# Kernel optimization log

Measured on AMD Instinct MI355X. Metric: run time of the kernel, lower is better.

The kernel has to match this reference:

```python
import jax, jax.numpy as jnp
import numpy as np

N, E, F_IN, HID, L, G = 50000, 400000, 128, 64, 3, 512
HEADS = 4  # per-head dim C = HID = 64 (PyG TransformerConv: out_channels per head)


def setup_inputs() -> dict:
    key = jax.random.key(0)
    ks = jax.random.split(key, 16)
    x = jax.random.normal(ks[0], (N, F_IN), dtype=jnp.float32)
    edge_index = jax.random.randint(ks[1], (2, E), 0, N, dtype=jnp.int64)
    batch = jnp.sort(jax.random.randint(ks[2], (N,), 0, G, dtype=jnp.int64))
    s_in = 1.0 / np.sqrt(F_IN)
    s_h = 1.0 / np.sqrt(HID)
    lin0_w = jax.random.normal(ks[3], (F_IN, HID), dtype=jnp.float32) * s_in
    lin0_b = jnp.zeros((HID,), dtype=jnp.float32)
    # stacked per-layer params [L, ...]
    Wq = jax.random.normal(ks[4], (L, HID, HEADS * HID), dtype=jnp.float32) * s_h
    Wk = jax.random.normal(ks[5], (L, HID, HEADS * HID), dtype=jnp.float32) * s_h
    Wv = jax.random.normal(ks[6], (L, HID, HEADS * HID), dtype=jnp.float32) * s_h
    bq = jnp.zeros((L, HEADS * HID), dtype=jnp.float32)
    bk = jnp.zeros((L, HEADS * HID), dtype=jnp.float32)
    bv = jnp.zeros((L, HEADS * HID), dtype=jnp.float32)
    Ws = jax.random.normal(ks[7], (L, HID, HID), dtype=jnp.float32) * s_h
    bs = jnp.zeros((L, HID), dtype=jnp.float32)
    return {"x": x, "edge_index": edge_index, "batch": batch,
            "lin0_w": lin0_w, "lin0_b": lin0_b,
            "Wq": Wq, "bq": bq, "Wk": Wk, "bk": bk, "Wv": Wv, "bv": bv,
            "Ws": Ws, "bs": bs}


def _transformer_conv(h, src, dst, Wq, bq, Wk, bk, Wv, bv, Ws, bs):
    n = h.shape[0]
    C = Wq.shape[1] // HEADS
    q = (h @ Wq + bq).reshape(n, HEADS, C)
    k = (h @ Wk + bk).reshape(n, HEADS, C)
    v = (h @ Wv + bv).reshape(n, HEADS, C)
    # per-edge attention logits: query at dst, key at src  -> [E, H]
    scale = jnp.asarray(1.0 / np.sqrt(C), h.dtype)
    logits = jnp.einsum('ehc,ehc->eh', q[dst], k[src]) * scale
    # segment softmax over incoming edges of each destination node
    m = jax.ops.segment_max(logits, dst, num_segments=n)
    e = jnp.exp(logits - m[dst])
    denom = jax.ops.segment_sum(e, dst, num_segments=n)
    p = e / denom[dst]  # every edge's dst segment is nonempty
    agg = jax.ops.segment_sum(p[:, :, None] * v[src], dst, num_segments=n)  # [n,H,C]
    return agg.mean(axis=1) + h @ Ws + bs  # concat=False: head mean + root skip


def reference(x, edge_index, batch, lin0_w, lin0_b, Wq, bq, Wk, bk, Wv, bv, Ws, bs):
    src, dst = edge_index[0], edge_index[1]
    h = x @ lin0_w + lin0_b  # [N, HID]; dropout is identity in eval mode
    for l in range(L):
        h = jax.nn.relu(_transformer_conv(h, src, dst, Wq[l], bq[l], Wk[l], bk[l],
                                          Wv[l], bv[l], Ws[l], bs[l]))
    # global add pool over graphs
    return jax.ops.segment_sum(h, batch, num_segments=G)  # [G, HID]
```

## Files before the change

### kernel.cpp

```cpp
#include <hip/hip_runtime.h>
#include <math.h>

#define F_IN 128
#define HID 64
#define NLAYER 3
#define QSW 832
#define QS_ROW 320
#define KV_ROW 512

typedef unsigned short ushort_t;
typedef __bf16 bf16x8 __attribute__((ext_vector_type(8)));
typedef unsigned short u16x8 __attribute__((ext_vector_type(8)));
typedef float f32x4 __attribute__((ext_vector_type(4)));
typedef float f32x2 __attribute__((ext_vector_type(2)));

__device__ __forceinline__ ushort_t f2bf(float f) {
  unsigned u = __float_as_uint(f);
  u += 0x7fffu + ((u >> 16) & 1u);
  return (ushort_t)(u >> 16);
}
__device__ __forceinline__ float bf2f(ushort_t s) {
  return __uint_as_float(((unsigned)s) << 16);
}
__device__ __forceinline__ float blo(unsigned u) { return __uint_as_float(u << 16); }
__device__ __forceinline__ float bhi(unsigned u) { return __uint_as_float(u & 0xffff0000u); }

__device__ __forceinline__ void dec8v(unsigned lo, unsigned hi, f32x2* f) {
  f[0] = __builtin_amdgcn_cvt_pk_f32_fp8((int)lo, false);
  f[1] = __builtin_amdgcn_cvt_pk_f32_fp8((int)lo, true);
  f[2] = __builtin_amdgcn_cvt_pk_f32_fp8((int)hi, false);
  f[3] = __builtin_amdgcn_cvt_pk_f32_fp8((int)hi, true);
}

__global__ __launch_bounds__(256) void aux_k(const int* __restrict__ dst, int* __restrict__ cnt,
                                             int* __restrict__ rank, int e, int nbE,
                                             const float* __restrict__ Wq, const float* __restrict__ Wk,
                                             const float* __restrict__ Wv, const float* __restrict__ Ws,
                                             const float* __restrict__ w0, const float* __restrict__ b0,
                                             const float* __restrict__ bq, const float* __restrict__ bk,
                                             const float* __restrict__ bv, const float* __restrict__ bs,
                                             ushort_t* __restrict__ wp0, ushort_t* __restrict__ wp12,
                                             float* __restrict__ bp,
                                             float* __restrict__ out, int out_size) {
  __shared__ float w0s[128 * 64];
  int blk = blockIdx.x;
  int t = threadIdx.x;
  if (blk < 105) {
    int b = blk * 4 + (t >> 6);
    int lane = t & 63;
    if (blk < 52) {
#pragma unroll
      for (int i = 0; i < 8; i++) {
        int idx = (t + i * 256) * 4;
        *(float4*)&w0s[idx] = *(const float4*)(w0 + idx);
      }
      __syncthreads();
      int ntg = b >> 2, kt = b & 3;
      int col = ntg * 16 + (lane & 15);
      int kb = kt * 32 + (lane >> 4) * 8;
      const float* W; int c, stride;
      if (col < 256)      { W = Wq; c = col;       stride = 256; }
      else if (col < 512) { W = Wk; c = col - 256; stride = 256; }
      else if (col < 768) { W = Wv; c = col - 512; stride = 256; }
      else                { W = Ws; c = col - 768; stride = 64; }
      float vals[8] = {0.f, 0.f, 0.f, 0.f, 0.f, 0.f, 0.f, 0.f};
#pragma unroll 4
      for (int j = 0; j < 64; j++) {
        float wj = W[(long long)j * stride + c];
#pragma unroll
        for (int ee = 0; ee < 8; ee++) vals[ee] = fmaf(w0s[(kb + ee) * 64 + j], wj, vals[ee]);
      }
      ushort_t* p = wp0 + ((long long)b * 64 + lane) * 8;
      ushort4 lo{f2bf(vals[0]), f2bf(vals[1]), f2bf(vals[2]), f2bf(vals[3])};
      ushort4 hi{f2bf(vals[4]), f2bf(vals[5]), f2bf(vals[6]), f2bf(vals[7])};
      *(ushort4*)p = lo;
      *(ushort4*)(p + 4) = hi;
    } else if (b < 416) {
      int idx = b - 208;
      int l = 1 + idx / 104, tt = idx % 104;
      int ntg = tt >> 1, kt = tt & 1;
      int col = ntg * 16 + (lane & 15);
      int kb = kt * 32 + (lane >> 4) * 8;
      const float* W; int c, stride;
      if (col < 256)      { W = Wq + (long long)l * 64 * 256; c = col;       stride = 256; }
      else if (col < 512) { W = Wk + (long long)l * 64 * 256; c = col - 256; stride = 256; }
      else if (col < 768) { W = Wv + (long long)l * 64 * 256; c = col - 512; stride = 256; }
      else                { W = Ws + (long long)l * 64 * 64;  c = col - 768; stride = 64; }
      float vals[8];
#pragma unroll
      for (int ee = 0; ee < 8; ee++) vals[ee] = W[(long long)(kb + ee) * stride + c];
      ushort_t* p = wp12 + (long long)(l - 1) * (104 * 512) + ((long long)tt * 64 + lane) * 8;
      ushort4 lo{f2bf(vals[0]), f2bf(vals[1]), f2bf(vals[2]), f2bf(vals[3])};
      ushort4 hi{f2bf(vals[4]), f2bf(vals[5]), f2bf(vals[6]), f2bf(vals[7])};
      *(ushort4*)p = lo;
      *(ushort4*)(p + 4) = hi;
    } else if (b < 419) {
      int l = b - 416;
      if (l == 0) {
        float b0v = b0[lane];
        for (int c = lane; c < QSW; c += 64) {
          const float* W; const float* borig; int cc, stride;
          if (c < 256)      { W = Wq; borig = bq; cc = c;       stride = 256; }
          else if (c < 512) { W = Wk; borig = bk; cc = c - 256; stride = 256; }
          else if (c < 768) { W = Wv; borig = bv; cc = c - 512; stride = 256; }
          else              { W = Ws; borig = bs; cc = c - 768; stride = 64; }
          float acc = borig[cc];
#pragma unroll 4
          for (int j = 0; j < 64; j++)
            acc = fmaf(__shfl(b0v, j), W[(long long)j * stride + cc], acc);
          bp[c] = acc;
        }
      } else {
        for (int c = lane; c < QSW; c += 64) {
          float v = (c < 256) ? bq[l * 256 + c]
                  : (c < 512) ? bk[l * 256 + c - 256]
                  : (c < 768) ? bv[l * 256 + c - 512]
                  : bs[l * 64 + c - 768];
          bp[l * QSW + c] = v;
        }
      }
    }
    return;
  }
  blk -= 105;
  if (blk < nbE) {
    int i = blk * 256 + t;
    if (i < e) rank[i] = atomicAdd(&cnt[dst[i]], 1);
    return;
  }
  blk -= nbE;
  int zi = blk * 256 + t;
  if (zi * 4 + 3 < out_size) {
    *(float4*)(out + zi * 4) = float4{0.f, 0.f, 0.f, 0.f};
  } else {
    for (int c = zi * 4; c < out_size; c++) out[c] = 0.f;
  }
}

__global__ __launch_bounds__(1024) void scan_block_k(const int* __restrict__ cnt, int* __restrict__ excl,
                                                     int* __restrict__ bsum, int n) {
  __shared__ int wsum[16];
  int t = threadIdx.x;
  int wv = t >> 6, lane = t & 63;
  int i = blockIdx.x * 1024 + t;
  int orig = (i < n) ? cnt[i] : 0;
  int v = orig;
#pragma unroll
  for (int off = 1; off < 64; off <<= 1) {
    int u = __shfl_up(v, off);
    if (lane >= off) v += u;
  }
  if (lane == 63) wsum[wv] = v;
  __syncthreads();
  if (t < 16) {
    int s = wsum[t];
    int s2 = s;
#pragma unroll
    for (int off = 1; off < 16; off <<= 1) {
      int u = __shfl_up(s2, off);
      if (t >= off) s2 += u;
    }
    wsum[t] = s2 - s;
  }
  __syncthreads();
  int base = wsum[wv];
  if (i < n) excl[i] = base + v - orig;
  if (t == 1023) bsum[blockIdx.x] = base + v;
}

__global__ __launch_bounds__(256) void scatter_rowptr_k(const int* __restrict__ src, const int* __restrict__ dst,
                                                        const int* __restrict__ excl, const int* __restrict__ bsum,
                                                        const int* __restrict__ rank, int* __restrict__ rowp,
                                                        int* __restrict__ srt, int n, int e, int nb) {
  __shared__ int sb[64];
  int t = threadIdx.x;
  if (t < 64) {
    int orig = (t < nb) ? bsum[t] : 0;
    int v = orig;
#pragma unroll
    for (int off = 1; off < 64; off <<= 1) {
      int u = __shfl_up(v, off);
      if (t >= off) v += u;
    }
    sb[t] = v - orig;
  }
  __syncthreads();
  int i = blockIdx.x * 256 + t;
  if (i < n) rowp[i] = excl[i] + sb[i >> 10];
  if (i == 0) rowp[n] = e;
  if (i < e) {
    int d = dst[i];
    srt[excl[d] + sb[d >> 10] + rank[i]] = src[i];
  }
}

#define QS_STR 328
#define KV_STR 528
template <int K, int AF32>
__global__ __launch_bounds__(256) void gemm_fused(const void* __restrict__ Av, const ushort_t* __restrict__ Wp,
                                                  const float* __restrict__ bias, ushort_t* __restrict__ Cq,
                                                  unsigned char* __restrict__ Ckv, int n) {
  constexpr int KT = K / 32;
  __shared__ ushort_t qs_lds[32][QS_STR];
  __shared__ unsigned char kv_lds[32][KV_STR];
  int tid = threadIdx.x;
  int lane = tid & 63;
  int wv = __builtin_amdgcn_readfirstlane((int)(tid >> 6));
  int m0 = blockIdx.x * 32;
  int lr = lane & 15, lq = lane >> 4;

  bf16x8 a[2][KT];
#pragma unroll
  for (int mr = 0; mr < 2; mr++) {
    int row = m0 + mr * 16 + lr;
    if (row >= n) row = n - 1;
    if constexpr (AF32) {
      const float* Af = (const float*)Av;
#pragma unroll
      for (int kt = 0; kt < KT; kt++) {
        const float* p = Af + (long long)row * K + kt * 32 + lq * 8;
        float4 f0 = *(const float4*)p;
        float4 f1 = *(const float4*)(p + 4);
        u16x8 u;
        u[0] = f2bf(f0.x); u[1] = f2bf(f0.y); u[2] = f2bf(f0.z); u[3] = f2bf(f0.w);
        u[4] = f2bf(f1.x); u[5] = f2bf(f1.y); u[6] = f2bf(f1.z); u[7] = f2bf(f1.w);
        a[mr][kt] = __builtin_bit_cast(bf16x8, u);
      }
    } else {
      const ushort_t* Ab = (const ushort_t*)Av;
#pragma unroll
      for (int kt = 0; kt < KT; kt++)
        a[mr][kt] = *(const bf16x8*)(Ab + (long long)row * K + kt * 32 + lq * 8);
    }
  }
  int ntg0 = wv * 13;
  bf16x8 bw[KT];
  bf16x8 bwn[KT];
#pragma unroll
  for (int kt = 0; kt < KT; kt++)
    bw[kt] = *(const bf16x8*)(Wp + ((long long)(ntg0 * KT + kt) * 64 + lane) * 8);
  float4 b4 = *(const float4*)(bias + ntg0 * 16 + lq * 4);
#pragma unroll 1
  for (int t = 0; t < 13; t++) {
    int ntg = ntg0 + t;
    float4 b4n;
    if (t < 12) {
#pragma unroll
      for (int kt = 0; kt < KT; kt++)
        bwn[kt] = *(const bf16x8*)(Wp + ((long long)((ntg + 1) * KT + kt) * 64 + lane) * 8);
      b4n = *(const float4*)(bias + (ntg + 1) * 16 + lq * 4);
    }
    f32x4 acc0 = {b4.x, b4.y, b4.z, b4.w};
    f32x4 acc1 = acc0;
#pragma unroll
    for (int kt = 0; kt < KT; kt++) {
      acc0 = __builtin_amdgcn_mfma_f32_16x16x32_bf16(bw[kt], a[0][kt], acc0, 0, 0, 0);
      acc1 = __builtin_amdgcn_mfma_f32_16x16x32_bf16(bw[kt], a[1][kt], acc1, 0, 0, 0);
    }
    if (ntg < 16) {
      int c = ntg * 16 + lq * 4;
      ushort4 o0{f2bf(acc0[0]), f2bf(acc0[1]), f2bf(acc0[2]), f2bf(acc0[3])};
      ushort4 o1{f2bf(acc1[0]), f2bf(acc1[1]), f2bf(acc1[2]), f2bf(acc1[3])};
      *(ushort4*)&qs_lds[lr][c] = o0;
      *(ushort4*)&qs_lds[16 + lr][c] = o1;
    } else if (ntg < 48) {
      bool isK = ntg < 32;
      int c = (isK ? (ntg - 16) : (ntg - 32)) * 16 + lq * 4;
      int pos = ((c >> 3) << 4) + (isK ? 0 : 8) + (c & 7);
      int p0 = __builtin_amdgcn_cvt_pk_fp8_f32(acc0[0], acc0[1], 0, false);
      p0 = __builtin_amdgcn_cvt_pk_fp8_f32(acc0[2], acc0[3], p0, true);
      int p1 = __builtin_amdgcn_cvt_pk_fp8_f32(acc1[0], acc1[1], 0, false);
      p1 = __builtin_amdgcn_cvt_pk_fp8_f32(acc1[2], acc1[3], p1, true);
      *(unsigned*)&kv_lds[lr][pos] = (unsigned)p0;
      *(unsigned*)&kv_lds[16 + lr][pos] = (unsigned)p1;
    } else {
      int c = 256 + (ntg - 48) * 16 + lq * 4;
      ushort4 o0{f2bf(acc0[0]), f2bf(acc0[1]), f2bf(acc0[2]), f2bf(acc0[3])};
      ushort4 o1{f2bf(acc1[0]), f2bf(acc1[1]), f2bf(acc1[2]), f2bf(acc1[3])};
      *(ushort4*)&qs_lds[lr][c] = o0;
      *(ushort4*)&qs_lds[16 + lr][c] = o1;
    }
#pragma unroll
    for (int kt = 0; kt < KT; kt++) bw[kt] = bwn[kt];
    b4 = b4n;
  }
  __syncthreads();
  int rows_here = n - m0;
  if (rows_here > 32) rows_here = 32;
  const char* qsl = (const char*)qs_lds;
  char* qout = (char*)Cq + (long long)m0 * (QS_ROW * 2);
#pragma unroll 1
  for (int off = tid * 16; off < 32 * 640; off += 4096) {
    int row = off / 640;
    if (row >= rows_here) break;
    int col = off - row * 640;
    uint4 v = *(const uint4*)(qsl + row * (QS_STR * 2) + col);
    *(uint4*)(qout + off) = v;
  }
  const char* kvl = (const char*)kv_lds;
  char* kout = (char*)Ckv + (long long)m0 * KV_ROW;
#pragma unroll 1
  for (int off = tid * 16; off < 32 * 512; off += 4096) {
    int row = off >> 9;
    if (row >= rows_here) break;
    int col = off & 511;
    uint4 v = *(const uint4*)(kvl + row * KV_STR + col);
    *(uint4*)(kout + off) = v;
  }
}

__global__ __launch_bounds__(256) void attn_k(const ushort_t* __restrict__ qs,
                                              const unsigned char* __restrict__ kv,
                                              const int* __restrict__ rowp, const int* __restrict__ srt,
                                              ushort_t* __restrict__ hn, int n) {
  int wvv = __builtin_amdgcn_readfirstlane((int)(threadIdx.x >> 6));
  int node = blockIdx.x * 4 + wvv;
  if (node >= n) return;
  int lane = threadIdx.x & 63;
  int half = lane >> 5;
  int sl = lane & 31;
  const uint4 qu = *(const uint4*)(qs + (long long)node * QS_ROW + sl * 8);
  f32x2 qf[4];
  qf[0] = f32x2{blo(qu.x), bhi(qu.x)} * 0.125f;
  qf[1] = f32x2{blo(qu.y), bhi(qu.y)} * 0.125f;
  qf[2] = f32x2{blo(qu.z), bhi(qu.z)} * 0.125f;
  qf[3] = f32x2{blo(qu.w), bhi(qu.w)} * 0.125f;
  int rs = rowp[node], re = rowp[node + 1];
  int last = re - 1;
  unsigned nm1 = (unsigned)(n - 1);
  float m = -INFINITY, d = 0.f;
  f32x2 a2[4];
#pragma unroll
  for (int j = 0; j < 4; j++) a2[j] = f32x2{0.f, 0.f};

  for (int i = rs; i < re; i += 8) {
    int b0 = i + half * 4;
    unsigned i0 = min((unsigned)srt[b0], nm1);
    unsigned i1 = min((unsigned)srt[b0 + 1], nm1);
    unsigned i2 = min((unsigned)srt[b0 + 2], nm1);
    unsigned i3 = min((unsigned)srt[b0 + 3], nm1);
    uint4 u0 = *(const uint4*)(kv + (long long)i0 * KV_ROW + sl * 16);
    uint4 u1 = *(const uint4*)(kv + (long long)i1 * KV_ROW + sl * 16);
    uint4 u2 = *(const uint4*)(kv + (long long)i2 * KV_ROW + sl * 16);
    uint4 u3 = *(const uint4*)(kv + (long long)i3 * KV_ROW + sl * 16);
    f32x2 kf0[4], kf1[4], kf2[4], kf3[4];
    dec8v(u0.x, u0.y, kf0); dec8v(u1.x, u1.y, kf1);
    dec8v(u2.x, u2.y, kf2); dec8v(u3.x, u3.y, kf3);
    f32x2 s0 = qf[0] * kf0[0], s1 = qf[0] * kf1[0], s2 = qf[0] * kf2[0], s3 = qf[0] * kf3[0];
#pragma unroll
    for (int j = 1; j < 4; j++) {
      s0 = s0 + qf[j] * kf0[j];
      s1 = s1 + qf[j] * kf1[j];
      s2 = s2 + qf[j] * kf2[j];
      s3 = s3 + qf[j] * kf3[j];
    }
    float t0 = s0[0] + s0[1], t1 = s1[0] + s1[1], t2 = s2[0] + s2[1], t3 = s3[0] + s3[1];
    t0 += __shfl_xor(t0, 1); t1 += __shfl_xor(t1, 1); t2 += __shfl_xor(t2, 1); t3 += __shfl_xor(t3, 1);
    t0 += __shfl_xor(t0, 2); t1 += __shfl_xor(t1, 2); t2 += __shfl_xor(t2, 2); t3 += __shfl_xor(t3, 2);
    t0 += __shfl_xor(t0, 4); t1 += __shfl_xor(t1, 4); t2 += __shfl_xor(t2, 4); t3 += __shfl_xor(t3, 4);
    if (b0 > last) t0 = -INFINITY;
    if (b0 + 1 > last) t1 = -INFINITY;
    if (b0 + 2 > last) t2 = -INFINITY;
    if (b0 + 3 > last) t3 = -INFINITY;
    float lm = fmaxf(fmaxf(t0, t1), fmaxf(t2, t3));
    lm = fmaxf(lm, __shfl_xor(lm, 32));
    if (__any(lm > m + 8.f)) {
      float mn = fmaxf(m, lm);
      float co = __expf(m - mn);
      d *= co;
#pragma unroll
      for (int j = 0; j < 4; j++) a2[j] = a2[j] * co;
      m = mn;
    }
    float p0e = __expf(t0 - m), p1e = __expf(t1 - m), p2e = __expf(t2 - m), p3e = __expf(t3 - m);
    d += (p0e + p1e) + (p2e + p3e);
    f32x2 vf0[4], vf1[4], vf2[4], vf3[4];
    dec8v(u0.z, u0.w, vf0); dec8v(u1.z, u1.w, vf1);
    dec8v(u2.z, u2.w, vf2); dec8v(u3.z, u3.w, vf3);
    f32x2 pe0 = {p0e, p0e}, pe1 = {p1e, p1e}, pe2 = {p2e, p2e}, pe3 = {p3e, p3e};
#pragma unroll
    for (int j = 0; j < 4; j++)
      a2[j] = a2[j] + (pe0 * vf0[j] + pe1 * vf1[j]) + (pe2 * vf2[j] + pe3 * vf3[j]);
  }
  d += __shfl_xor(d, 32);
  float a[8];
#pragma unroll
  for (int j = 0; j < 4; j++) {
    a[2 * j] = a2[j][0] + __shfl_xor(a2[j][0], 32);
    a[2 * j + 1] = a2[j][1] + __shfl_xor(a2[j][1], 32);
  }
  float inv = (d > 0.f) ? 1.f / d : 0.f;
  float r[8];
#pragma unroll
  for (int j = 0; j < 8; j++) {
    r[j] = a[j] * inv;
    r[j] += __shfl_xor(r[j], 8);
    r[j] += __shfl_xor(r[j], 16);
  }
  if (lane < 8) {
    const u16x8 s8 = *(const u16x8*)(qs + (long long)node * QS_ROW + 256 + lane * 8);
    u16x8 o;
#pragma unroll
    for (int j = 0; j < 8; j++)
      o[j] = f2bf(fmaxf(r[j] * 0.25f + bf2f(s8[j]), 0.f));
    *(u16x8*)(hn + (long long)node * HID + lane * 8) = o;
  }
}

#define POOL_NPB 128
__global__ __launch_bounds__(64) void pool_k(const ushort_t* __restrict__ h, const int* __restrict__ batch,
                                             float* __restrict__ out, int n) {
  int c = threadIdx.x;
  int n0 = blockIdx.x * POOL_NPB;
  int n1 = n0 + POOL_NPB;
  if (n1 > n) n1 = n;
  if (n0 >= n) return;
  float acc = 0.f;
  int g = batch[n0];
  for (int node = n0; node < n1; node++) {
    int gb = batch[node];
    if (gb != g) {
      atomicAdd(&out[g * 64 + c], acc);
      acc = 0.f;
      g = gb;
    }
    acc += bf2f(h[(long long)node * 64 + c]);
  }
  atomicAdd(&out[g * 64 + c], acc);
}

extern "C" void kernel_launch(void* const* d_in, const int* in_sizes, int n_in,
                              void* d_out, int out_size, void* d_ws, size_t ws_size,
                              hipStream_t stream) {
  const float* x  = (const float*)d_in[0];
  const int* ei   = (const int*)d_in[1];
  const int* batch = (const int*)d_in[2];
  const float* w0 = (const float*)d_in[3];
  const float* b0 = (const float*)d_in[4];
  const float* Wq = (const float*)d_in[5];
  const float* bq = (const float*)d_in[6];
  const float* Wk = (const float*)d_in[7];
  const float* bk = (const float*)d_in[8];
  const float* Wv = (const float*)d_in[9];
  const float* bv = (const float*)d_in[10];
  const float* Ws = (const float*)d_in[11];
  const float* bs = (const float*)d_in[12];
  int N = in_sizes[0] / F_IN;
  int E = in_sizes[1] / 2;
  const int* esrc = ei;
  const int* edst = ei + E;

  float* bp = (float*)d_ws;
  unsigned char* kvb = (unsigned char*)(bp + 3 * QSW);
  ushort_t* ha = (ushort_t*)(kvb + (size_t)N * KV_ROW);
  ushort_t* hb = ha + (long long)N * HID;
  ushort_t* qs = hb + (long long)N * HID;
  ushort_t* wp0  = qs + (long long)N * QS_ROW;
  ushort_t* wp12 = wp0 + 208 * 512;
  int* cnt  = (int*)(wp12 + 2 * 104 * 512);
  int* excl = cnt + N;
  int* rowp = excl + N;
  int* bsum = rowp + N + 1;
  int* rank = bsum + 64;
  int* srt  = rank + E;

  int nbE = (E + 255) / 256;
  int sbBlocks = (N + 1023) / 1024;
  int nzBlocks = (out_size / 4 + 255) / 256;

  hipMemsetAsync(cnt, 0, (size_t)N * sizeof(int), stream);
  aux_k<<<105 + nbE + nzBlocks, 256, 0, stream>>>(edst, cnt, rank, E, nbE,
                                                  Wq, Wk, Wv, Ws, w0, b0, bq, bk, bv, bs,
                                                  wp0, wp12, bp, (float*)d_out, out_size);
  scan_block_k<<<sbBlocks, 1024, 0, stream>>>(cnt, excl, bsum, N);
  scatter_rowptr_k<<<nbE, 256, 0, stream>>>(esrc, edst, excl, bsum, rank, rowp, srt, N, E, sbBlocks);

  int gBlocks = (N + 31) / 32;

  gemm_fused<128, 1><<<gBlocks, 256, 0, stream>>>(x, wp0, bp, qs, kvb, N);
  attn_k<<<(N + 3) / 4, 256, 0, stream>>>(qs, kvb, rowp, srt, ha, N);
  gemm_fused<64, 0><<<gBlocks, 256, 0, stream>>>(ha, wp12, bp + QSW, qs, kvb, N);
  attn_k<<<(N + 3) / 4, 256, 0, stream>>>(qs, kvb, rowp, srt, hb, N);
  gemm_fused<64, 0><<<gBlocks, 256, 0, stream>>>(hb, wp12 + 104 * 512, bp + 2 * QSW, qs, kvb, N);
  attn_k<<<(N + 3) / 4, 256, 0, stream>>>(qs, kvb, rowp, srt, ha, N);

  pool_k<<<(N + POOL_NPB - 1) / POOL_NPB, 64, 0, stream>>>(ha, batch, (float*)d_out, N);
}
```

Before: 324.8 us.

## Split aux kernel into histogram and weight-pack kernels with 4-wave pack reduction

The combined aux kernel, which did weight packing, the edge histogram/rank and output zeroing, is split into a simple histogram kernel and a separate pack kernel. The pack kernel now uses one block per tile and spreads each 64-long dot product across all four waves, reducing the partial sums through LDS. The long serial dot products in the old aux blocks could stall that launch, so this shortens the critical path. Output zeroing moves to a memset before pooling, which adds launches and therefore extra launch overhead.

```diff
diff --git a/kernel.cpp b/kernel.cpp
--- a/kernel.cpp
+++ b/kernel.cpp
@@ -32,109 +32,10 @@
   f[3] = __builtin_amdgcn_cvt_pk_f32_fp8((int)hi, true);
 }
 
-__global__ __launch_bounds__(256) void aux_k(const int* __restrict__ dst, int* __restrict__ cnt,
-                                             int* __restrict__ rank, int e, int nbE,
-                                             const float* __restrict__ Wq, const float* __restrict__ Wk,
-                                             const float* __restrict__ Wv, const float* __restrict__ Ws,
-                                             const float* __restrict__ w0, const float* __restrict__ b0,
-                                             const float* __restrict__ bq, const float* __restrict__ bk,
-                                             const float* __restrict__ bv, const float* __restrict__ bs,
-                                             ushort_t* __restrict__ wp0, ushort_t* __restrict__ wp12,
-                                             float* __restrict__ bp,
-                                             float* __restrict__ out, int out_size) {
-  __shared__ float w0s[128 * 64];
-  int blk = blockIdx.x;
-  int t = threadIdx.x;
-  if (blk < 105) {
-    int b = blk * 4 + (t >> 6);
-    int lane = t & 63;
-    if (blk < 52) {
-#pragma unroll
-      for (int i = 0; i < 8; i++) {
-        int idx = (t + i * 256) * 4;
-        *(float4*)&w0s[idx] = *(const float4*)(w0 + idx);
-      }
-      __syncthreads();
-      int ntg = b >> 2, kt = b & 3;
-      int col = ntg * 16 + (lane & 15);
-      int kb = kt * 32 + (lane >> 4) * 8;
-      const float* W; int c, stride;
-      if (col < 256)      { W = Wq; c = col;       stride = 256; }
-      else if (col < 512) { W = Wk; c = col - 256; stride = 256; }
-      else if (col < 768) { W = Wv; c = col - 512; stride = 256; }
-      else                { W = Ws; c = col - 768; stride = 64; }
-      float vals[8] = {0.f, 0.f, 0.f, 0.f, 0.f, 0.f, 0.f, 0.f};
-#pragma unroll 4
-      for (int j = 0; j < 64; j++) {
-        float wj = W[(long long)j * stride + c];
-#pragma unroll
-        for (int ee = 0; ee < 8; ee++) vals[ee] = fmaf(w0s[(kb + ee) * 64 + j], wj, vals[ee]);
-      }
-      ushort_t* p = wp0 + ((long long)b * 64 + lane) * 8;
-      ushort4 lo{f2bf(vals[0]), f2bf(vals[1]), f2bf(vals[2]), f2bf(vals[3])};
-      ushort4 hi{f2bf(vals[4]), f2bf(vals[5]), f2bf(vals[6]), f2bf(vals[7])};
-      *(ushort4*)p = lo;
-      *(ushort4*)(p + 4) = hi;
-    } else if (b < 416) {
-      int idx = b - 208;
-      int l = 1 + idx / 104, tt = idx % 104;
-      int ntg = tt >> 1, kt = tt & 1;
-      int col = ntg * 16 + (lane & 15);
-      int kb = kt * 32 + (lane >> 4) * 8;
-      const float* W; int c, stride;
-      if (col < 256)      { W = Wq + (long long)l * 64 * 256; c = col;       stride = 256; }
-      else if (col < 512) { W = Wk + (long long)l * 64 * 256; c = col - 256; stride = 256; }
-      else if (col < 768) { W = Wv + (long long)l * 64 * 256; c = col - 512; stride = 256; }
-      else                { W = Ws + (long long)l * 64 * 64;  c = col - 768; stride = 64; }
-      float vals[8];
-#pragma unroll
-      for (int ee = 0; ee < 8; ee++) vals[ee] = W[(long long)(kb + ee) * stride + c];
-      ushort_t* p = wp12 + (long long)(l - 1) * (104 * 512) + ((long long)tt * 64 + lane) * 8;
-      ushort4 lo{f2bf(vals[0]), f2bf(vals[1]), f2bf(vals[2]), f2bf(vals[3])};
-      ushort4 hi{f2bf(vals[4]), f2bf(vals[5]), f2bf(vals[6]), f2bf(vals[7])};
-      *(ushort4*)p = lo;
-      *(ushort4*)(p + 4) = hi;
-    } else if (b < 419) {
-      int l = b - 416;
-      if (l == 0) {
-        float b0v = b0[lane];
-        for (int c = lane; c < QSW; c += 64) {
-          const float* W; const float* borig; int cc, stride;
-          if (c < 256)      { W = Wq; borig = bq; cc = c;       stride = 256; }
-          else if (c < 512) { W = Wk; borig = bk; cc = c - 256; stride = 256; }
-          else if (c < 768) { W = Wv; borig = bv; cc = c - 512; stride = 256; }
-          else              { W = Ws; borig = bs; cc = c - 768; stride = 64; }
-          float acc = borig[cc];
-#pragma unroll 4
-          for (int j = 0; j < 64; j++)
-            acc = fmaf(__shfl(b0v, j), W[(long long)j * stride + cc], acc);
-          bp[c] = acc;
-        }
-      } else {
-        for (int c = lane; c < QSW; c += 64) {
-          float v = (c < 256) ? bq[l * 256 + c]
-                  : (c < 512) ? bk[l * 256 + c - 256]
-                  : (c < 768) ? bv[l * 256 + c - 512]
-                  : bs[l * 64 + c - 768];
-          bp[l * QSW + c] = v;
-        }
-      }
-    }
-    return;
-  }
-  blk -= 105;
-  if (blk < nbE) {
-    int i = blk * 256 + t;
-    if (i < e) rank[i] = atomicAdd(&cnt[dst[i]], 1);
-    return;
-  }
-  blk -= nbE;
-  int zi = blk * 256 + t;
-  if (zi * 4 + 3 < out_size) {
-    *(float4*)(out + zi * 4) = float4{0.f, 0.f, 0.f, 0.f};
-  } else {
-    for (int c = zi * 4; c < out_size; c++) out[c] = 0.f;
-  }
+__global__ __launch_bounds__(256) void hist_rank_k(const int* __restrict__ dst, int* __restrict__ cnt,
+                                                   int* __restrict__ rank, int e) {
+  int i = blockIdx.x * 256 + threadIdx.x;
+  if (i < e) rank[i] = atomicAdd(&cnt[dst[i]], 1);
 }
 
 __global__ __launch_bounds__(1024) void scan_block_k(const int* __restrict__ cnt, int* __restrict__ excl,
@@ -191,6 +92,106 @@
   if (i < e) {
     int d = dst[i];
     srt[excl[d] + sb[d >> 10] + rank[i]] = src[i];
+  }
+}
+
+__global__ __launch_bounds__(256) void pack2_k(const float* __restrict__ Wq, const float* __restrict__ Wk,
+                                               const float* __restrict__ Wv, const float* __restrict__ Ws,
+                                               const float* __restrict__ w0, const float* __restrict__ b0,
+                                               const float* __restrict__ bq, const float* __restrict__ bk,
+                                               const float* __restrict__ bv, const float* __restrict__ bs,
+                                               ushort_t* __restrict__ wp0, ushort_t* __restrict__ wp12,
+                                               float* __restrict__ bp) {
+  __shared__ float w0s[32 * 64];
+  __shared__ float part[3][64][8];
+  int b = blockIdx.x;
+  int t = threadIdx.x;
+  int wv = t >> 6, lane = t & 63;
+  if (b < 208) {
+    int ntg = b >> 2, kt = b & 3;
+    {
+      int base = kt * 32 * 64;
+      int idx = t * 8;
+      *(float4*)&w0s[idx] = *(const float4*)(w0 + base + idx);
+      *(float4*)&w0s[idx + 4] = *(const float4*)(w0 + base + idx + 4);
+    }
+    __syncthreads();
+    int col = ntg * 16 + (lane & 15);
+    int kbl = (lane >> 4) * 8;
+    const float* W; int c, stride;
+    if (col < 256)      { W = Wq; c = col;       stride = 256; }
+    else if (col < 512) { W = Wk; c = col - 256; stride = 256; }
+    else if (col < 768) { W = Wv; c = col - 512; stride = 256; }
+    else                { W = Ws; c = col - 768; stride = 64; }
+    float vals[8] = {0.f, 0.f, 0.f, 0.f, 0.f, 0.f, 0.f, 0.f};
+#pragma unroll 4
+    for (int jj = 0; jj < 16; jj++) {
+      int j = wv * 16 + jj;
+      float wj = W[(long long)j * stride + c];
+#pragma unroll
+      for (int ee = 0; ee < 8; ee++) vals[ee] = fmaf(w0s[(kbl + ee) * 64 + j], wj, vals[ee]);
+    }
+    if (wv > 0) {
+#pragma unroll
+      for (int ee = 0; ee < 8; ee++) part[wv - 1][lane][ee] = vals[ee];
+    }
+    __syncthreads();
+    if (wv == 0) {
+#pragma unroll
+      for (int ee = 0; ee < 8; ee++)
+        vals[ee] += part[0][lane][ee] + part[1][lane][ee] + part[2][lane][ee];
+      ushort_t* p = wp0 + ((long long)b * 64 + lane) * 8;
+      ushort4 lo{f2bf(vals[0]), f2bf(vals[1]), f2bf(vals[2]), f2bf(vals[3])};
+      ushort4 hi{f2bf(vals[4]), f2bf(vals[5]), f2bf(vals[6]), f2bf(vals[7])};
+      *(ushort4*)p = lo;
+      *(ushort4*)(p + 4) = hi;
+    }
+  } else if (b < 416) {
+    if (wv != 0) return;
+    int idx = b - 208;
+    int l = 1 + idx / 104, tt = idx % 104;
+    int ntg = tt >> 1, kt = tt & 1;
+    int col = ntg * 16 + (lane & 15);
+    int kb = kt * 32 + (lane >> 4) * 8;
+    const float* W; int c, stride;
+    if (col < 256)      { W = Wq + (long long)l * 64 * 256; c = col;       stride = 256; }
+    else if (col < 512) { W = Wk + (long long)l * 64 * 256; c = col - 256; stride = 256; }
+    else if (col < 768) { W = Wv + (long long)l * 64 * 256; c = col - 512; stride = 256; }
+    else                { W = Ws + (long long)l * 64 * 64;  c = col - 768; stride = 64; }
+    float vals[8];
+#pragma unroll
+    for (int ee = 0; ee < 8; ee++) vals[ee] = W[(long long)(kb + ee) * stride + c];
+    ushort_t* p = wp12 + (long long)(l - 1) * (104 * 512) + ((long long)tt * 64 + lane) * 8;
+    ushort4 lo{f2bf(vals[0]), f2bf(vals[1]), f2bf(vals[2]), f2bf(vals[3])};
+    ushort4 hi{f2bf(vals[4]), f2bf(vals[5]), f2bf(vals[6]), f2bf(vals[7])};
+    *(ushort4*)p = lo;
+    *(ushort4*)(p + 4) = hi;
+  } else {
+    if (wv != 0) return;
+    int l = b - 416;
+    if (l == 0) {
+      float b0v = b0[lane];
+      for (int c = lane; c < QSW; c += 64) {
+        const float* W; const float* borig; int cc, stride;
+        if (c < 256)      { W = Wq; borig = bq; cc = c;       stride = 256; }
+        else if (c < 512) { W = Wk; borig = bk; cc = c - 256; stride = 256; }
+        else if (c < 768) { W = Wv; borig = bv; cc = c - 512; stride = 256; }
+        else              { W = Ws; borig = bs; cc = c - 768; stride = 64; }
+        float acc = borig[cc];
+#pragma unroll 4
+        for (int j = 0; j < 64; j++)
+          acc = fmaf(__shfl(b0v, j), W[(long long)j * stride + cc], acc);
+        bp[c] = acc;
+      }
+    } else {
+      for (int c = lane; c < QSW; c += 64) {
+        float v = (c < 256) ? bq[l * 256 + c]
+                : (c < 512) ? bk[l * 256 + c - 256]
+                : (c < 768) ? bv[l * 256 + c - 512]
+                : bs[l * 64 + c - 768];
+        bp[l * QSW + c] = v;
+      }
+    }
   }
 }
 
@@ -466,14 +467,13 @@
 
   int nbE = (E + 255) / 256;
   int sbBlocks = (N + 1023) / 1024;
-  int nzBlocks = (out_size / 4 + 255) / 256;
 
   hipMemsetAsync(cnt, 0, (size_t)N * sizeof(int), stream);
-  aux_k<<<105 + nbE + nzBlocks, 256, 0, stream>>>(edst, cnt, rank, E, nbE,
-                                                  Wq, Wk, Wv, Ws, w0, b0, bq, bk, bv, bs,
-                                                  wp0, wp12, bp, (float*)d_out, out_size);
+  hist_rank_k<<<nbE, 256, 0, stream>>>(edst, cnt, rank, E);
   scan_block_k<<<sbBlocks, 1024, 0, stream>>>(cnt, excl, bsum, N);
   scatter_rowptr_k<<<nbE, 256, 0, stream>>>(esrc, edst, excl, bsum, rank, rowp, srt, N, E, sbBlocks);
+
+  pack2_k<<<419, 256, 0, stream>>>(Wq, Wk, Wv, Ws, w0, b0, bq, bk, bv, bs, wp0, wp12, bp);
 
   int gBlocks = (N + 31) / 32;
 
@@ -484,5 +484,6 @@
   gemm_fused<64, 0><<<gBlocks, 256, 0, stream>>>(hb, wp12 + 104 * 512, bp + 2 * QSW, qs, kvb, N);
   attn_k<<<(N + 3) / 4, 256, 0, stream>>>(qs, kvb, rowp, srt, ha, N);
 
+  hipMemsetAsync(d_out, 0, (size_t)out_size * sizeof(float), stream);
   pool_k<<<(N + POOL_NPB - 1) / POOL_NPB, 64, 0, stream>>>(ha, batch, (float*)d_out, N);
 }
```

New measurement: 308.6 us (median of 2 runs). 5.0% less time.
